# Performance work log

Hardware: AMD Instinct MI355X
Metric: run time of the kernel (lower is better)

Reference implementation:

```python
import jax, jax.numpy as jnp
import numpy as np

N_NODES = 50000
N_EDGES = 800000
D_IN = 128
D_HID = 128
D_OUT = 2


def setup_inputs() -> dict:
    key = jax.random.key(0)
    ks = jax.random.split(key, 8)
    x = jax.random.normal(ks[0], (N_NODES, D_IN), dtype=jnp.float32)
    edge_index = jax.random.randint(ks[1], (2, N_EDGES), 0, N_NODES, dtype=jnp.int64)
    s = 0.05
    W1_l = jax.random.normal(ks[2], (D_HID, D_IN), dtype=jnp.float32) * s
    W1_r = jax.random.normal(ks[3], (D_HID, D_IN), dtype=jnp.float32) * s
    b1 = jax.random.normal(ks[4], (D_HID,), dtype=jnp.float32) * s
    W2_l = jax.random.normal(ks[5], (D_OUT, D_HID), dtype=jnp.float32) * s
    W2_r = jax.random.normal(ks[6], (D_OUT, D_HID), dtype=jnp.float32) * s
    b2 = jax.random.normal(ks[7], (D_OUT,), dtype=jnp.float32) * s
    return {"x": x, "edge_index": edge_index, "W1_l": W1_l, "W1_r": W1_r,
            "b1": b1, "W2_l": W2_l, "W2_r": W2_r, "b2": b2}


def _sage_conv(x, src, dst, W_l, W_r, b):
    # mean-aggregate neighbor features: gather from src, scatter-sum to dst
    n = x.shape[0]
    msg = x[src]                                            # [E, d]
    agg = jax.ops.segment_sum(msg, dst, num_segments=n)      # [n, d]
    cnt = jax.ops.segment_sum(jnp.ones((src.shape[0],), x.dtype), dst,
                              num_segments=n)
    agg = agg / jnp.maximum(cnt, 1.0)[:, None]
    # lin_l(aggregated) + lin_r(self) + bias  (PyG SAGEConv with root_weight)
    return agg @ W_l.T + x @ W_r.T + b


def reference(x, edge_index, W1_l, W1_r, b1, W2_l, W2_r, b2):
    src, dst = edge_index[0], edge_index[1]
    h = _sage_conv(x, src, dst, W1_l, W1_r, b1)
    h = jax.nn.relu(h)
    out = _sage_conv(h, src, dst, W2_l, W2_r, b2)
    return out
```

## Files before the change

kernel.cpp:

```cpp
#include <hip/hip_runtime.h>

#define N_NODES 50000
#define N_EDGES 800000
#define CAP 64

typedef __bf16 bf16_8 __attribute__((ext_vector_type(8)));
typedef float  f32_4  __attribute__((ext_vector_type(4)));
typedef unsigned short u16;


__global__ void prep_kernel(const float* __restrict__ W1l, const float* __restrict__ W1r,
                            __bf16* __restrict__ Wt, const float* __restrict__ x,
                            __bf16* __restrict__ xb, const int* __restrict__ src,
                            const int* __restrict__ dst,
                            int* __restrict__ deg_p, u16* __restrict__ bins) {
    int b = blockIdx.x;
    if (b < 1563) {
        int t = b * 256 + threadIdx.x;
        if (t < 400000) {
            int d0 = dst[t],          s0 = src[t];
            int d1 = dst[t + 400000], s1 = src[t + 400000];
            int p0 = atomicAdd(&deg_p[d0 * 16], 1);
            int p1 = atomicAdd(&deg_p[d1 * 16], 1);
            {
                int node = t >> 4, c8 = t & 15;
                const float4* xp = (const float4*)(x + node * 128 + c8 * 8);
                float4 v0 = xp[0], v1 = xp[1];
                bf16_8 o;
                o[0] = (__bf16)v0.x; o[1] = (__bf16)v0.y; o[2] = (__bf16)v0.z; o[3] = (__bf16)v0.w;
                o[4] = (__bf16)v1.x; o[5] = (__bf16)v1.y; o[6] = (__bf16)v1.z; o[7] = (__bf16)v1.w;
                *(bf16_8*)(xb + t * 8) = o;
            }
            {
                int t2 = t + 400000;
                int node = t2 >> 4, c8 = t2 & 15;
                const float4* xp = (const float4*)(x + node * 128 + c8 * 8);
                float4 v0 = xp[0], v1 = xp[1];
                bf16_8 o;
                o[0] = (__bf16)v0.x; o[1] = (__bf16)v0.y; o[2] = (__bf16)v0.z; o[3] = (__bf16)v0.w;
                o[4] = (__bf16)v1.x; o[5] = (__bf16)v1.y; o[6] = (__bf16)v1.z; o[7] = (__bf16)v1.w;
                *(bf16_8*)(xb + t2 * 8) = o;
            }
            if (p0 < CAP) bins[d0 * CAP + p0] = (u16)s0;
            if (p1 < CAP) bins[d1 * CAP + p1] = (u16)s1;
        }
    } else {
        int t = (b - 1563) * 256 + threadIdx.x;
        int n = t >> 8, k = t & 255;
        float v = (k < 128) ? W1l[n * 128 + k] : W1r[n * 128 + (k - 128)];
        Wt[t] = (__bf16)v;
    }
}

#define LDA 264
__global__ __launch_bounds__(256) void gather_gemm_kernel(
    const int* __restrict__ deg_p, const u16* __restrict__ bins,
    const __bf16* __restrict__ xb, const __bf16* __restrict__ Wt,
    const float* __restrict__ b1, const float* __restrict__ W2l,
    const float* __restrict__ W2r, float* __restrict__ y, float* __restrict__ z)
{
    __shared__ __bf16 As[16 * LDA];
    __shared__ float4 sp[4][16];

    const int i0 = blockIdx.x * 16;
    const int tid = threadIdx.x;
    const int row = tid >> 4, c8 = tid & 15;
    const int gi = i0 + row;

    bf16_8 sv = *(const bf16_8*)(xb + gi * 128 + c8 * 8);
    *(bf16_8*)(&As[row * LDA + 128 + c8 * 8]) = sv;

    {
        const u16* bp = bins + gi * CAP;
        int n = min(deg_p[gi * 16], CAP);
        float acc[8] = {};
        int j = 0;
        for (; j + 8 <= n; j += 8) {
            int idx[8];
            #pragma unroll
            for (int u = 0; u < 8; ++u) idx[u] = bp[j + u];
            bf16_8 vv[8];
            #pragma unroll
            for (int u = 0; u < 8; ++u)
                vv[u] = *(const bf16_8*)(xb + idx[u] * 128 + c8 * 8);
            #pragma unroll
            for (int u = 0; u < 8; ++u) {
                float s01 = (float)vv[0][u] + (float)vv[1][u];
                float s23 = (float)vv[2][u] + (float)vv[3][u];
                float s45 = (float)vv[4][u] + (float)vv[5][u];
                float s67 = (float)vv[6][u] + (float)vv[7][u];
                acc[u] += (s01 + s23) + (s45 + s67);
            }
        }
        for (; j + 2 <= n; j += 2) {
            int s0 = bp[j], s1 = bp[j + 1];
            bf16_8 v0 = *(const bf16_8*)(xb + s0 * 128 + c8 * 8);
            bf16_8 v1 = *(const bf16_8*)(xb + s1 * 128 + c8 * 8);
            #pragma unroll
            for (int u = 0; u < 8; ++u) acc[u] += (float)v0[u] + (float)v1[u];
        }
        if (j < n) {
            int s0 = bp[j];
            bf16_8 v0 = *(const bf16_8*)(xb + s0 * 128 + c8 * 8);
            #pragma unroll
            for (int u = 0; u < 8; ++u) acc[u] += (float)v0[u];
        }
        float inv = 1.0f / fmaxf((float)n, 1.0f);
        bf16_8 o;
        #pragma unroll
        for (int u = 0; u < 8; ++u) o[u] = (__bf16)(acc[u] * inv);
        *(bf16_8*)(&As[row * LDA + c8 * 8]) = o;
    }
    __syncthreads();

    const int wv = tid >> 6, lane = tid & 63;
    const int mr = lane & 15, q = lane >> 4;
    const int n0 = wv * 2, n1 = wv * 2 + 1;

    f32_4 acc0 = (f32_4){0.f,0.f,0.f,0.f}, acc1 = (f32_4){0.f,0.f,0.f,0.f};
    #pragma unroll
    for (int ks = 0; ks < 8; ++ks) {
        bf16_8 a  = *(const bf16_8*)(&As[mr * LDA + ks * 32 + q * 8]);
        bf16_8 b0 = *(const bf16_8*)(Wt + (n0 * 16 + mr) * 256 + ks * 32 + q * 8);
        bf16_8 bb = *(const bf16_8*)(Wt + (n1 * 16 + mr) * 256 + ks * 32 + q * 8);
        acc0 = __builtin_amdgcn_mfma_f32_16x16x32_bf16(a, b0, acc0, 0, 0, 0);
        acc1 = __builtin_amdgcn_mfma_f32_16x16x32_bf16(a, bb, acc1, 0, 0, 0);
    }

    float py0[4] = {}, py1[4] = {}, pz0[4] = {}, pz1[4] = {};
    #pragma unroll
    for (int ntl = 0; ntl < 2; ++ntl) {
        int col = (wv * 2 + ntl) * 16 + mr;
        f32_4 a = ntl ? acc1 : acc0;
        float bb  = b1[col];
        float wl0 = W2l[col], wl1 = W2l[128 + col];
        float wr0 = W2r[col], wr1 = W2r[128 + col];
        #pragma unroll
        for (int r = 0; r < 4; ++r) {
            float hv = fmaxf(a[r] + bb, 0.f);
            py0[r] += hv * wl0; py1[r] += hv * wl1;
            pz0[r] += hv * wr0; pz1[r] += hv * wr1;
        }
    }
    #pragma unroll
    for (int off = 1; off < 16; off <<= 1) {
        #pragma unroll
        for (int r = 0; r < 4; ++r) {
            py0[r] += __shfl_xor(py0[r], off);
            py1[r] += __shfl_xor(py1[r], off);
            pz0[r] += __shfl_xor(pz0[r], off);
            pz1[r] += __shfl_xor(pz1[r], off);
        }
    }
    if (mr < 4) {
        int r = mr;
        sp[wv][q * 4 + r] = make_float4(py0[r], py1[r], pz0[r], pz1[r]);
    }
    __syncthreads();

    if (tid < 16) {
        float4 a0 = sp[0][tid], a1 = sp[1][tid], a2 = sp[2][tid], a3 = sp[3][tid];
        ((float2*)y)[i0 + tid] = make_float2(a0.x + a1.x + a2.x + a3.x,
                                             a0.y + a1.y + a2.y + a3.y);
        ((float2*)z)[i0 + tid] = make_float2(a0.z + a1.z + a2.z + a3.z,
                                             a0.w + a1.w + a2.w + a3.w);
    }
}

__global__ void final_kernel(const int* __restrict__ deg_p, const u16* __restrict__ bins,
                             const float* __restrict__ y, const float* __restrict__ z,
                             const float* __restrict__ b2, float* __restrict__ out) {
    int t = blockIdx.x * 256 + threadIdx.x;
    int node = t >> 4, p = t & 15;
    const u16* bp = bins + node * CAP;
    int n = min(deg_p[node * 16], CAP);
    float a0 = 0.f, a1 = 0.f;
    for (int j = p; j < n; j += 16) {
        float2 v = ((const float2*)y)[bp[j]];
        a0 += v.x; a1 += v.y;
    }
    a0 += __shfl_xor(a0, 1); a1 += __shfl_xor(a1, 1);
    a0 += __shfl_xor(a0, 2); a1 += __shfl_xor(a1, 2);
    a0 += __shfl_xor(a0, 4); a1 += __shfl_xor(a1, 4);
    a0 += __shfl_xor(a0, 8); a1 += __shfl_xor(a1, 8);
    if (p == 0) {
        float inv = 1.0f / fmaxf((float)n, 1.0f);
        float2 zz = ((const float2*)z)[node];
        ((float2*)out)[node] = make_float2(a0 * inv + zz.x + b2[0],
                                           a1 * inv + zz.y + b2[1]);
    }
}

extern "C" void kernel_launch(void* const* d_in, const int* in_sizes, int n_in,
                              void* d_out, int out_size, void* d_ws, size_t ws_size,
                              hipStream_t stream) {
    const float* x   = (const float*)d_in[0];
    const int*   ei  = (const int*)  d_in[1];
    const float* W1l = (const float*)d_in[2];
    const float* W1r = (const float*)d_in[3];
    const float* b1  = (const float*)d_in[4];
    const float* W2l = (const float*)d_in[5];
    const float* W2r = (const float*)d_in[6];
    const float* b2  = (const float*)d_in[7];
    float* out = (float*)d_out;
    const int* src = ei;
    const int* dst = ei + N_EDGES;

    char* ws = (char*)d_ws;
    int*    deg_p = (int*)   (ws + 0);
    u16*    bins  = (u16*)   (ws + 3200000);
    __bf16* xb    = (__bf16*)(ws + 9600000);
    float*  y     = (float*) (ws + 22400000);
    float*  z     = (float*) (ws + 22800000);
    __bf16* Wt    = (__bf16*)(ws + 23200000);

    hipMemsetAsync(deg_p, 0, 3200000, stream);
    prep_kernel<<<1691, 256, 0, stream>>>(W1l, W1r, Wt, x, xb, src, dst, deg_p, bins);
    gather_gemm_kernel<<<3125, 256, 0, stream>>>(deg_p, bins, xb, Wt, b1, W2l, W2r, y, z);
    final_kernel<<<3125, 256, 0, stream>>>(deg_p, bins, y, z, b2, out);
}
```

Baseline: 184.7 us.

## Fuse memset and three kernels into one cooperative persistent kernel with grid syncs

Replaces the memset plus prep, gather-GEMM and final kernels with a single cooperative kernel that steps through the phases separated by grid.sync, using grid-stride loops and a persistent tile loop. The aim is to remove launch overhead and inter-kernel gaps. In exchange it adds grid-wide barriers, caps occupancy at the cooperative grid size (at most 2048 blocks), and the gather phase now runs with fewer concurrent blocks, which may hide less memory latency.

```diff
diff --git a/kernel.cpp b/kernel.cpp
--- a/kernel.cpp
+++ b/kernel.cpp
@@ -1,193 +1,182 @@
 #include <hip/hip_runtime.h>
+#include <hip/hip_cooperative_groups.h>
+
+namespace cg = cooperative_groups;
 
 #define N_NODES 50000
 #define N_EDGES 800000
 #define CAP 64
+#define N_TILES 3125
+#define LDA 264
 
 typedef __bf16 bf16_8 __attribute__((ext_vector_type(8)));
 typedef float  f32_4  __attribute__((ext_vector_type(4)));
 typedef unsigned short u16;
 
 
-__global__ void prep_kernel(const float* __restrict__ W1l, const float* __restrict__ W1r,
-                            __bf16* __restrict__ Wt, const float* __restrict__ x,
-                            __bf16* __restrict__ xb, const int* __restrict__ src,
-                            const int* __restrict__ dst,
-                            int* __restrict__ deg_p, u16* __restrict__ bins) {
-    int b = blockIdx.x;
-    if (b < 1563) {
-        int t = b * 256 + threadIdx.x;
-        if (t < 400000) {
-            int d0 = dst[t],          s0 = src[t];
-            int d1 = dst[t + 400000], s1 = src[t + 400000];
-            int p0 = atomicAdd(&deg_p[d0 * 16], 1);
-            int p1 = atomicAdd(&deg_p[d1 * 16], 1);
-            {
-                int node = t >> 4, c8 = t & 15;
-                const float4* xp = (const float4*)(x + node * 128 + c8 * 8);
-                float4 v0 = xp[0], v1 = xp[1];
-                bf16_8 o;
-                o[0] = (__bf16)v0.x; o[1] = (__bf16)v0.y; o[2] = (__bf16)v0.z; o[3] = (__bf16)v0.w;
-                o[4] = (__bf16)v1.x; o[5] = (__bf16)v1.y; o[6] = (__bf16)v1.z; o[7] = (__bf16)v1.w;
-                *(bf16_8*)(xb + t * 8) = o;
-            }
-            {
-                int t2 = t + 400000;
-                int node = t2 >> 4, c8 = t2 & 15;
-                const float4* xp = (const float4*)(x + node * 128 + c8 * 8);
-                float4 v0 = xp[0], v1 = xp[1];
-                bf16_8 o;
-                o[0] = (__bf16)v0.x; o[1] = (__bf16)v0.y; o[2] = (__bf16)v0.z; o[3] = (__bf16)v0.w;
-                o[4] = (__bf16)v1.x; o[5] = (__bf16)v1.y; o[6] = (__bf16)v1.z; o[7] = (__bf16)v1.w;
-                *(bf16_8*)(xb + t2 * 8) = o;
-            }
-            if (p0 < CAP) bins[d0 * CAP + p0] = (u16)s0;
-            if (p1 < CAP) bins[d1 * CAP + p1] = (u16)s1;
-        }
-    } else {
-        int t = (b - 1563) * 256 + threadIdx.x;
+__global__ __launch_bounds__(256, 7) void mega_kernel(
+    const float* __restrict__ x, const int* __restrict__ src, const int* __restrict__ dst,
+    const float* __restrict__ W1l, const float* __restrict__ W1r, const float* __restrict__ b1,
+    const float* __restrict__ W2l, const float* __restrict__ W2r, const float* __restrict__ b2,
+    float* __restrict__ out, int* __restrict__ deg_p, u16* __restrict__ bins,
+    __bf16* __restrict__ xb, float* __restrict__ y, float* __restrict__ z,
+    __bf16* __restrict__ Wt)
+{
+    cg::grid_group grid = cg::this_grid();
+    __shared__ __bf16 As[16 * LDA];
+    __shared__ float4 sp[4][16];
+
+    const int tid  = threadIdx.x;
+    const int gsz  = gridDim.x * 256;
+    const int gtid = blockIdx.x * 256 + tid;
+
+    for (int i = gtid; i < N_NODES; i += gsz) deg_p[i * 16] = 0;
+    grid.sync();
+
+    for (int t = gtid; t < N_EDGES; t += gsz) {
+        int d = dst[t], s = src[t];
+        int pos = atomicAdd(&deg_p[d * 16], 1);
+        int node = t >> 4, c8 = t & 15;
+        const float4* xp = (const float4*)(x + node * 128 + c8 * 8);
+        float4 v0 = xp[0], v1 = xp[1];
+        bf16_8 o;
+        o[0] = (__bf16)v0.x; o[1] = (__bf16)v0.y; o[2] = (__bf16)v0.z; o[3] = (__bf16)v0.w;
+        o[4] = (__bf16)v1.x; o[5] = (__bf16)v1.y; o[6] = (__bf16)v1.z; o[7] = (__bf16)v1.w;
+        *(bf16_8*)(xb + t * 8) = o;
+        if (pos < CAP) bins[d * CAP + pos] = (u16)s;
+    }
+    for (int t = gtid; t < 128 * 256; t += gsz) {
         int n = t >> 8, k = t & 255;
         float v = (k < 128) ? W1l[n * 128 + k] : W1r[n * 128 + (k - 128)];
         Wt[t] = (__bf16)v;
     }
-}
-
-#define LDA 264
-__global__ __launch_bounds__(256) void gather_gemm_kernel(
-    const int* __restrict__ deg_p, const u16* __restrict__ bins,
-    const __bf16* __restrict__ xb, const __bf16* __restrict__ Wt,
-    const float* __restrict__ b1, const float* __restrict__ W2l,
-    const float* __restrict__ W2r, float* __restrict__ y, float* __restrict__ z)
-{
-    __shared__ __bf16 As[16 * LDA];
-    __shared__ float4 sp[4][16];
-
-    const int i0 = blockIdx.x * 16;
-    const int tid = threadIdx.x;
+    grid.sync();
+
     const int row = tid >> 4, c8 = tid & 15;
-    const int gi = i0 + row;
-
-    bf16_8 sv = *(const bf16_8*)(xb + gi * 128 + c8 * 8);
-    *(bf16_8*)(&As[row * LDA + 128 + c8 * 8]) = sv;
-
-    {
-        const u16* bp = bins + gi * CAP;
-        int n = min(deg_p[gi * 16], CAP);
-        float acc[8] = {};
-        int j = 0;
-        for (; j + 8 <= n; j += 8) {
-            int idx[8];
-            #pragma unroll
-            for (int u = 0; u < 8; ++u) idx[u] = bp[j + u];
-            bf16_8 vv[8];
-            #pragma unroll
-            for (int u = 0; u < 8; ++u)
-                vv[u] = *(const bf16_8*)(xb + idx[u] * 128 + c8 * 8);
-            #pragma unroll
-            for (int u = 0; u < 8; ++u) {
-                float s01 = (float)vv[0][u] + (float)vv[1][u];
-                float s23 = (float)vv[2][u] + (float)vv[3][u];
-                float s45 = (float)vv[4][u] + (float)vv[5][u];
-                float s67 = (float)vv[6][u] + (float)vv[7][u];
-                acc[u] += (s01 + s23) + (s45 + s67);
-            }
-        }
-        for (; j + 2 <= n; j += 2) {
-            int s0 = bp[j], s1 = bp[j + 1];
-            bf16_8 v0 = *(const bf16_8*)(xb + s0 * 128 + c8 * 8);
-            bf16_8 v1 = *(const bf16_8*)(xb + s1 * 128 + c8 * 8);
-            #pragma unroll
-            for (int u = 0; u < 8; ++u) acc[u] += (float)v0[u] + (float)v1[u];
-        }
-        if (j < n) {
-            int s0 = bp[j];
-            bf16_8 v0 = *(const bf16_8*)(xb + s0 * 128 + c8 * 8);
-            #pragma unroll
-            for (int u = 0; u < 8; ++u) acc[u] += (float)v0[u];
-        }
-        float inv = 1.0f / fmaxf((float)n, 1.0f);
-        bf16_8 o;
-        #pragma unroll
-        for (int u = 0; u < 8; ++u) o[u] = (__bf16)(acc[u] * inv);
-        *(bf16_8*)(&As[row * LDA + c8 * 8]) = o;
-    }
-    __syncthreads();
-
     const int wv = tid >> 6, lane = tid & 63;
     const int mr = lane & 15, q = lane >> 4;
     const int n0 = wv * 2, n1 = wv * 2 + 1;
 
-    f32_4 acc0 = (f32_4){0.f,0.f,0.f,0.f}, acc1 = (f32_4){0.f,0.f,0.f,0.f};
-    #pragma unroll
-    for (int ks = 0; ks < 8; ++ks) {
-        bf16_8 a  = *(const bf16_8*)(&As[mr * LDA + ks * 32 + q * 8]);
-        bf16_8 b0 = *(const bf16_8*)(Wt + (n0 * 16 + mr) * 256 + ks * 32 + q * 8);
-        bf16_8 bb = *(const bf16_8*)(Wt + (n1 * 16 + mr) * 256 + ks * 32 + q * 8);
-        acc0 = __builtin_amdgcn_mfma_f32_16x16x32_bf16(a, b0, acc0, 0, 0, 0);
-        acc1 = __builtin_amdgcn_mfma_f32_16x16x32_bf16(a, bb, acc1, 0, 0, 0);
-    }
-
-    float py0[4] = {}, py1[4] = {}, pz0[4] = {}, pz1[4] = {};
-    #pragma unroll
-    for (int ntl = 0; ntl < 2; ++ntl) {
-        int col = (wv * 2 + ntl) * 16 + mr;
-        f32_4 a = ntl ? acc1 : acc0;
-        float bb  = b1[col];
-        float wl0 = W2l[col], wl1 = W2l[128 + col];
-        float wr0 = W2r[col], wr1 = W2r[128 + col];
+    for (int tile = blockIdx.x; tile < N_TILES; tile += gridDim.x) {
+        const int i0 = tile * 16;
+        const int gi = i0 + row;
+
+        *(bf16_8*)(&As[row * LDA + 128 + c8 * 8]) =
+            *(const bf16_8*)(xb + gi * 128 + c8 * 8);
+
+        {
+            const u16* bp = bins + gi * CAP;
+            int n = min(deg_p[gi * 16], CAP);
+            float acc[8] = {};
+            int j = 0;
+            for (; j + 8 <= n; j += 8) {
+                int idx[8];
+                #pragma unroll
+                for (int u = 0; u < 8; ++u) idx[u] = bp[j + u];
+                bf16_8 vv[8];
+                #pragma unroll
+                for (int u = 0; u < 8; ++u)
+                    vv[u] = *(const bf16_8*)(xb + idx[u] * 128 + c8 * 8);
+                #pragma unroll
+                for (int u = 0; u < 8; ++u) {
+                    float s01 = (float)vv[0][u] + (float)vv[1][u];
+                    float s23 = (float)vv[2][u] + (float)vv[3][u];
+                    float s45 = (float)vv[4][u] + (float)vv[5][u];
+                    float s67 = (float)vv[6][u] + (float)vv[7][u];
+                    acc[u] += (s01 + s23) + (s45 + s67);
+                }
+            }
+            for (; j + 2 <= n; j += 2) {
+                int s0 = bp[j], s1 = bp[j + 1];
+                bf16_8 v0 = *(const bf16_8*)(xb + s0 * 128 + c8 * 8);
+                bf16_8 v1 = *(const bf16_8*)(xb + s1 * 128 + c8 * 8);
+                #pragma unroll
+                for (int u = 0; u < 8; ++u) acc[u] += (float)v0[u] + (float)v1[u];
+            }
+            if (j < n) {
+                int s0 = bp[j];
+                bf16_8 v0 = *(const bf16_8*)(xb + s0 * 128 + c8 * 8);
+                #pragma unroll
+                for (int u = 0; u < 8; ++u) acc[u] += (float)v0[u];
+            }
+            float inv = 1.0f / fmaxf((float)n, 1.0f);
+            bf16_8 o;
+            #pragma unroll
+            for (int u = 0; u < 8; ++u) o[u] = (__bf16)(acc[u] * inv);
+            *(bf16_8*)(&As[row * LDA + c8 * 8]) = o;
+        }
+        __syncthreads();
+
+        f32_4 acc0 = (f32_4){0.f,0.f,0.f,0.f}, acc1 = (f32_4){0.f,0.f,0.f,0.f};
         #pragma unroll
-        for (int r = 0; r < 4; ++r) {
-            float hv = fmaxf(a[r] + bb, 0.f);
-            py0[r] += hv * wl0; py1[r] += hv * wl1;
-            pz0[r] += hv * wr0; pz1[r] += hv * wr1;
-        }
-    }
-    #pragma unroll
-    for (int off = 1; off < 16; off <<= 1) {
+        for (int ks = 0; ks < 8; ++ks) {
+            bf16_8 a  = *(const bf16_8*)(&As[mr * LDA + ks * 32 + q * 8]);
+            bf16_8 b0 = *(const bf16_8*)(Wt + (n0 * 16 + mr) * 256 + ks * 32 + q * 8);
+            bf16_8 bb = *(const bf16_8*)(Wt + (n1 * 16 + mr) * 256 + ks * 32 + q * 8);
+            acc0 = __builtin_amdgcn_mfma_f32_16x16x32_bf16(a, b0, acc0, 0, 0, 0);
+            acc1 = __builtin_amdgcn_mfma_f32_16x16x32_bf16(a, bb, acc1, 0, 0, 0);
+        }
+
+        float py0[4] = {}, py1[4] = {}, pz0[4] = {}, pz1[4] = {};
         #pragma unroll
-        for (int r = 0; r < 4; ++r) {
-            py0[r] += __shfl_xor(py0[r], off);
-            py1[r] += __shfl_xor(py1[r], off);
-            pz0[r] += __shfl_xor(pz0[r], off);
-            pz1[r] += __shfl_xor(pz1[r], off);
-        }
-    }
-    if (mr < 4) {
-        int r = mr;
-        sp[wv][q * 4 + r] = make_float4(py0[r], py1[r], pz0[r], pz1[r]);
-    }
-    __syncthreads();
-
-    if (tid < 16) {
-        float4 a0 = sp[0][tid], a1 = sp[1][tid], a2 = sp[2][tid], a3 = sp[3][tid];
-        ((float2*)y)[i0 + tid] = make_float2(a0.x + a1.x + a2.x + a3.x,
-                                             a0.y + a1.y + a2.y + a3.y);
-        ((float2*)z)[i0 + tid] = make_float2(a0.z + a1.z + a2.z + a3.z,
-                                             a0.w + a1.w + a2.w + a3.w);
-    }
-}
-
-__global__ void final_kernel(const int* __restrict__ deg_p, const u16* __restrict__ bins,
-                             const float* __restrict__ y, const float* __restrict__ z,
-                             const float* __restrict__ b2, float* __restrict__ out) {
-    int t = blockIdx.x * 256 + threadIdx.x;
-    int node = t >> 4, p = t & 15;
-    const u16* bp = bins + node * CAP;
-    int n = min(deg_p[node * 16], CAP);
-    float a0 = 0.f, a1 = 0.f;
-    for (int j = p; j < n; j += 16) {
-        float2 v = ((const float2*)y)[bp[j]];
-        a0 += v.x; a1 += v.y;
-    }
-    a0 += __shfl_xor(a0, 1); a1 += __shfl_xor(a1, 1);
-    a0 += __shfl_xor(a0, 2); a1 += __shfl_xor(a1, 2);
-    a0 += __shfl_xor(a0, 4); a1 += __shfl_xor(a1, 4);
-    a0 += __shfl_xor(a0, 8); a1 += __shfl_xor(a1, 8);
-    if (p == 0) {
-        float inv = 1.0f / fmaxf((float)n, 1.0f);
-        float2 zz = ((const float2*)z)[node];
-        ((float2*)out)[node] = make_float2(a0 * inv + zz.x + b2[0],
-                                           a1 * inv + zz.y + b2[1]);
+        for (int ntl = 0; ntl < 2; ++ntl) {
+            int col = (wv * 2 + ntl) * 16 + mr;
+            f32_4 a = ntl ? acc1 : acc0;
+            float bb  = b1[col];
+            float wl0 = W2l[col], wl1 = W2l[128 + col];
+            float wr0 = W2r[col], wr1 = W2r[128 + col];
+            #pragma unroll
+            for (int r = 0; r < 4; ++r) {
+                float hv = fmaxf(a[r] + bb, 0.f);
+                py0[r] += hv * wl0; py1[r] += hv * wl1;
+                pz0[r] += hv * wr0; pz1[r] += hv * wr1;
+            }
+        }
+        #pragma unroll
+        for (int off = 1; off < 16; off <<= 1) {
+            #pragma unroll
+            for (int r = 0; r < 4; ++r) {
+                py0[r] += __shfl_xor(py0[r], off);
+                py1[r] += __shfl_xor(py1[r], off);
+                pz0[r] += __shfl_xor(pz0[r], off);
+                pz1[r] += __shfl_xor(pz1[r], off);
+            }
+        }
+        if (mr < 4) {
+            int r = mr;
+            sp[wv][q * 4 + r] = make_float4(py0[r], py1[r], pz0[r], pz1[r]);
+        }
+        __syncthreads();
+
+        if (tid < 16) {
+            float4 a0 = sp[0][tid], a1 = sp[1][tid], a2 = sp[2][tid], a3 = sp[3][tid];
+            ((float2*)y)[i0 + tid] = make_float2(a0.x + a1.x + a2.x + a3.x,
+                                                 a0.y + a1.y + a2.y + a3.y);
+            ((float2*)z)[i0 + tid] = make_float2(a0.z + a1.z + a2.z + a3.z,
+                                                 a0.w + a1.w + a2.w + a3.w);
+        }
+    }
+    grid.sync();
+
+    for (int t = gtid; t < 16 * N_NODES; t += gsz) {
+        int node = t >> 4, p = t & 15;
+        const u16* bp = bins + node * CAP;
+        int n = min(deg_p[node * 16], CAP);
+        float a0 = 0.f, a1 = 0.f;
+        for (int j = p; j < n; j += 16) {
+            float2 v = ((const float2*)y)[bp[j]];
+            a0 += v.x; a1 += v.y;
+        }
+        a0 += __shfl_xor(a0, 1); a1 += __shfl_xor(a1, 1);
+        a0 += __shfl_xor(a0, 2); a1 += __shfl_xor(a1, 2);
+        a0 += __shfl_xor(a0, 4); a1 += __shfl_xor(a1, 4);
+        a0 += __shfl_xor(a0, 8); a1 += __shfl_xor(a1, 8);
+        if (p == 0) {
+            float inv = 1.0f / fmaxf((float)n, 1.0f);
+            float2 zz = ((const float2*)z)[node];
+            ((float2*)out)[node] = make_float2(a0 * inv + zz.x + b2[0],
+                                               a1 * inv + zz.y + b2[1]);
+        }
     }
 }
 
@@ -214,8 +203,23 @@
     float*  z     = (float*) (ws + 22800000);
     __bf16* Wt    = (__bf16*)(ws + 23200000);
 
-    hipMemsetAsync(deg_p, 0, 3200000, stream);
-    prep_kernel<<<1691, 256, 0, stream>>>(W1l, W1r, Wt, x, xb, src, dst, deg_p, bins);
-    gather_gemm_kernel<<<3125, 256, 0, stream>>>(deg_p, bins, xb, Wt, b1, W2l, W2r, y, z);
-    final_kernel<<<3125, 256, 0, stream>>>(deg_p, bins, y, z, b2, out);
+    static int coopGrid = 0;
+    if (coopGrid == 0) {
+        int dev = 0;
+        hipGetDevice(&dev);
+        hipDeviceProp_t prop;
+        hipGetDeviceProperties(&prop, dev);
+        int mab = 0;
+        hipOccupancyMaxActiveBlocksPerMultiprocessor(&mab, (const void*)mega_kernel, 256, 0);
+        if (mab < 1) mab = 1;
+        coopGrid = mab * prop.multiProcessorCount;
+        if (coopGrid > 2048) coopGrid = 2048;
+    }
+
+    void* args[] = {(void*)&x, (void*)&src, (void*)&dst, (void*)&W1l, (void*)&W1r,
+                    (void*)&b1, (void*)&W2l, (void*)&W2r, (void*)&b2, (void*)&out,
+                    (void*)&deg_p, (void*)&bins, (void*)&xb, (void*)&y, (void*)&z,
+                    (void*)&Wt};
+    hipLaunchCooperativeKernel((const void*)mega_kernel, dim3(coopGrid), dim3(256),
+                               args, 0, stream);
 }
```

After: 459.5 us. 2.49x slower.

## Gather neighbor features from an FP8 copy of x instead of bf16

Applied to the files above, without the earlier changes.

The prep kernel now also writes an FP8-quantized copy of x, and the neighbor-mean gather in the first layer reads 8-byte FP8 chunks instead of 16-byte bf16 chunks. It also loads bin indices as packed vectors and has each prep thread handle four edges instead of two. This roughly halves the random-gather traffic, which dominates the first layer. The cost is an extra write of the FP8 array, more conversion instructions, and lower precision in the aggregated features, which could affect accuracy against tolerance.

```diff
diff --git a/kernel.cpp b/kernel.cpp
--- a/kernel.cpp
+++ b/kernel.cpp
@@ -7,45 +7,60 @@
 typedef __bf16 bf16_8 __attribute__((ext_vector_type(8)));
 typedef float  f32_4  __attribute__((ext_vector_type(4)));
 typedef unsigned short u16;
-
+typedef unsigned char  u8;
+
+
+__device__ __forceinline__ void f8cvt(int2 q, float f[8]) {
+    f[0] = __builtin_amdgcn_cvt_f32_fp8(q.x, 0);
+    f[1] = __builtin_amdgcn_cvt_f32_fp8(q.x, 1);
+    f[2] = __builtin_amdgcn_cvt_f32_fp8(q.x, 2);
+    f[3] = __builtin_amdgcn_cvt_f32_fp8(q.x, 3);
+    f[4] = __builtin_amdgcn_cvt_f32_fp8(q.y, 0);
+    f[5] = __builtin_amdgcn_cvt_f32_fp8(q.y, 1);
+    f[6] = __builtin_amdgcn_cvt_f32_fp8(q.y, 2);
+    f[7] = __builtin_amdgcn_cvt_f32_fp8(q.y, 3);
+}
 
 __global__ void prep_kernel(const float* __restrict__ W1l, const float* __restrict__ W1r,
                             __bf16* __restrict__ Wt, const float* __restrict__ x,
-                            __bf16* __restrict__ xb, const int* __restrict__ src,
-                            const int* __restrict__ dst,
+                            __bf16* __restrict__ xb, u8* __restrict__ xb8,
+                            const int* __restrict__ src, const int* __restrict__ dst,
                             int* __restrict__ deg_p, u16* __restrict__ bins) {
     int b = blockIdx.x;
-    if (b < 1563) {
+    if (b < 782) {
         int t = b * 256 + threadIdx.x;
-        if (t < 400000) {
+        if (t < 200000) {
             int d0 = dst[t],          s0 = src[t];
-            int d1 = dst[t + 400000], s1 = src[t + 400000];
+            int d1 = dst[t + 200000], s1 = src[t + 200000];
+            int d2 = dst[t + 400000], s2 = src[t + 400000];
+            int d3 = dst[t + 600000], s3 = src[t + 600000];
             int p0 = atomicAdd(&deg_p[d0 * 16], 1);
             int p1 = atomicAdd(&deg_p[d1 * 16], 1);
-            {
-                int node = t >> 4, c8 = t & 15;
+            int p2 = atomicAdd(&deg_p[d2 * 16], 1);
+            int p3 = atomicAdd(&deg_p[d3 * 16], 1);
+            #pragma unroll
+            for (int k = 0; k < 4; ++k) {
+                int c = t + k * 200000;
+                int node = c >> 4, c8 = c & 15;
                 const float4* xp = (const float4*)(x + node * 128 + c8 * 8);
                 float4 v0 = xp[0], v1 = xp[1];
                 bf16_8 o;
                 o[0] = (__bf16)v0.x; o[1] = (__bf16)v0.y; o[2] = (__bf16)v0.z; o[3] = (__bf16)v0.w;
                 o[4] = (__bf16)v1.x; o[5] = (__bf16)v1.y; o[6] = (__bf16)v1.z; o[7] = (__bf16)v1.w;
-                *(bf16_8*)(xb + t * 8) = o;
-            }
-            {
-                int t2 = t + 400000;
-                int node = t2 >> 4, c8 = t2 & 15;
-                const float4* xp = (const float4*)(x + node * 128 + c8 * 8);
-                float4 v0 = xp[0], v1 = xp[1];
-                bf16_8 o;
-                o[0] = (__bf16)v0.x; o[1] = (__bf16)v0.y; o[2] = (__bf16)v0.z; o[3] = (__bf16)v0.w;
-                o[4] = (__bf16)v1.x; o[5] = (__bf16)v1.y; o[6] = (__bf16)v1.z; o[7] = (__bf16)v1.w;
-                *(bf16_8*)(xb + t2 * 8) = o;
+                *(bf16_8*)(xb + c * 8) = o;
+                int lo = __builtin_amdgcn_cvt_pk_fp8_f32(v0.x, v0.y, 0, false);
+                lo     = __builtin_amdgcn_cvt_pk_fp8_f32(v0.z, v0.w, lo, true);
+                int hi = __builtin_amdgcn_cvt_pk_fp8_f32(v1.x, v1.y, 0, false);
+                hi     = __builtin_amdgcn_cvt_pk_fp8_f32(v1.z, v1.w, hi, true);
+                *(int2*)(xb8 + c * 8) = make_int2(lo, hi);
             }
             if (p0 < CAP) bins[d0 * CAP + p0] = (u16)s0;
             if (p1 < CAP) bins[d1 * CAP + p1] = (u16)s1;
+            if (p2 < CAP) bins[d2 * CAP + p2] = (u16)s2;
+            if (p3 < CAP) bins[d3 * CAP + p3] = (u16)s3;
         }
     } else {
-        int t = (b - 1563) * 256 + threadIdx.x;
+        int t = (b - 782) * 256 + threadIdx.x;
         int n = t >> 8, k = t & 255;
         float v = (k < 128) ? W1l[n * 128 + k] : W1r[n * 128 + (k - 128)];
         Wt[t] = (__bf16)v;
@@ -55,7 +70,8 @@
 #define LDA 264
 __global__ __launch_bounds__(256) void gather_gemm_kernel(
     const int* __restrict__ deg_p, const u16* __restrict__ bins,
-    const __bf16* __restrict__ xb, const __bf16* __restrict__ Wt,
+    const __bf16* __restrict__ xb, const u8* __restrict__ xb8,
+    const __bf16* __restrict__ Wt,
     const float* __restrict__ b1, const float* __restrict__ W2l,
     const float* __restrict__ W2r, float* __restrict__ y, float* __restrict__ z)
 {
@@ -76,34 +92,53 @@
         float acc[8] = {};
         int j = 0;
         for (; j + 8 <= n; j += 8) {
-            int idx[8];
-            #pragma unroll
-            for (int u = 0; u < 8; ++u) idx[u] = bp[j + u];
-            bf16_8 vv[8];
+            uint4 bq = *(const uint4*)(bp + j);
+            int2 q0 = *(const int2*)(xb8 + (bq.x & 0xffff) * 128 + c8 * 8);
+            int2 q1 = *(const int2*)(xb8 + (bq.x >> 16)    * 128 + c8 * 8);
+            int2 q2 = *(const int2*)(xb8 + (bq.y & 0xffff) * 128 + c8 * 8);
+            int2 q3 = *(const int2*)(xb8 + (bq.y >> 16)    * 128 + c8 * 8);
+            int2 q4 = *(const int2*)(xb8 + (bq.z & 0xffff) * 128 + c8 * 8);
+            int2 q5 = *(const int2*)(xb8 + (bq.z >> 16)    * 128 + c8 * 8);
+            int2 q6 = *(const int2*)(xb8 + (bq.w & 0xffff) * 128 + c8 * 8);
+            int2 q7 = *(const int2*)(xb8 + (bq.w >> 16)    * 128 + c8 * 8);
+            float f0[8], f1[8], f2[8], f3[8], f4[8], f5[8], f6[8], f7[8];
+            f8cvt(q0, f0); f8cvt(q1, f1); f8cvt(q2, f2); f8cvt(q3, f3);
+            f8cvt(q4, f4); f8cvt(q5, f5); f8cvt(q6, f6); f8cvt(q7, f7);
             #pragma unroll
             for (int u = 0; u < 8; ++u)
-                vv[u] = *(const bf16_8*)(xb + idx[u] * 128 + c8 * 8);
-            #pragma unroll
-            for (int u = 0; u < 8; ++u) {
-                float s01 = (float)vv[0][u] + (float)vv[1][u];
-                float s23 = (float)vv[2][u] + (float)vv[3][u];
-                float s45 = (float)vv[4][u] + (float)vv[5][u];
-                float s67 = (float)vv[6][u] + (float)vv[7][u];
-                acc[u] += (s01 + s23) + (s45 + s67);
-            }
-        }
-        for (; j + 2 <= n; j += 2) {
-            int s0 = bp[j], s1 = bp[j + 1];
-            bf16_8 v0 = *(const bf16_8*)(xb + s0 * 128 + c8 * 8);
-            bf16_8 v1 = *(const bf16_8*)(xb + s1 * 128 + c8 * 8);
-            #pragma unroll
-            for (int u = 0; u < 8; ++u) acc[u] += (float)v0[u] + (float)v1[u];
+                acc[u] += ((f0[u] + f1[u]) + (f2[u] + f3[u])) +
+                          ((f4[u] + f5[u]) + (f6[u] + f7[u]));
+        }
+        if (j + 4 <= n) {
+            uint2 bq = *(const uint2*)(bp + j);
+            int2 q0 = *(const int2*)(xb8 + (bq.x & 0xffff) * 128 + c8 * 8);
+            int2 q1 = *(const int2*)(xb8 + (bq.x >> 16)    * 128 + c8 * 8);
+            int2 q2 = *(const int2*)(xb8 + (bq.y & 0xffff) * 128 + c8 * 8);
+            int2 q3 = *(const int2*)(xb8 + (bq.y >> 16)    * 128 + c8 * 8);
+            float f0[8], f1[8], f2[8], f3[8];
+            f8cvt(q0, f0); f8cvt(q1, f1); f8cvt(q2, f2); f8cvt(q3, f3);
+            #pragma unroll
+            for (int u = 0; u < 8; ++u)
+                acc[u] += (f0[u] + f1[u]) + (f2[u] + f3[u]);
+            j += 4;
+        }
+        if (j + 2 <= n) {
+            int i0e = bp[j], i1e = bp[j + 1];
+            int2 q0 = *(const int2*)(xb8 + i0e * 128 + c8 * 8);
+            int2 q1 = *(const int2*)(xb8 + i1e * 128 + c8 * 8);
+            float f0[8], f1[8];
+            f8cvt(q0, f0); f8cvt(q1, f1);
+            #pragma unroll
+            for (int u = 0; u < 8; ++u) acc[u] += f0[u] + f1[u];
+            j += 2;
         }
         if (j < n) {
-            int s0 = bp[j];
-            bf16_8 v0 = *(const bf16_8*)(xb + s0 * 128 + c8 * 8);
-            #pragma unroll
-            for (int u = 0; u < 8; ++u) acc[u] += (float)v0[u];
+            int i0e = bp[j];
+            int2 q0 = *(const int2*)(xb8 + i0e * 128 + c8 * 8);
+            float f0[8];
+            f8cvt(q0, f0);
+            #pragma unroll
+            for (int u = 0; u < 8; ++u) acc[u] += f0[u];
         }
         float inv = 1.0f / fmaxf((float)n, 1.0f);
         bf16_8 o;
@@ -210,12 +245,13 @@
     int*    deg_p = (int*)   (ws + 0);
     u16*    bins  = (u16*)   (ws + 3200000);
     __bf16* xb    = (__bf16*)(ws + 9600000);
-    float*  y     = (float*) (ws + 22400000);
-    float*  z     = (float*) (ws + 22800000);
-    __bf16* Wt    = (__bf16*)(ws + 23200000);
+    u8*     xb8   = (u8*)    (ws + 22400000);
+    float*  y     = (float*) (ws + 28800000);
+    float*  z     = (float*) (ws + 29200000);
+    __bf16* Wt    = (__bf16*)(ws + 29600000);
 
     hipMemsetAsync(deg_p, 0, 3200000, stream);
-    prep_kernel<<<1691, 256, 0, stream>>>(W1l, W1r, Wt, x, xb, src, dst, deg_p, bins);
-    gather_gemm_kernel<<<3125, 256, 0, stream>>>(deg_p, bins, xb, Wt, b1, W2l, W2r, y, z);
+    prep_kernel<<<910, 256, 0, stream>>>(W1l, W1r, Wt, x, xb, xb8, src, dst, deg_p, bins);
+    gather_gemm_kernel<<<3125, 256, 0, stream>>>(deg_p, bins, xb, xb8, Wt, b1, W2l, W2r, y, z);
     final_kernel<<<3125, 256, 0, stream>>>(deg_p, bins, y, z, b2, out);
 }
```

After: 177.5 us. 3.9% less time.
